# Performance work log

Measured on AMD Instinct MI355X. Metric: run time of the kernel, lower is better.

The kernel has to match this reference:

```python
import jax, jax.numpy as jnp
import numpy as np

B, S, D = 64, 4096, 64          # bsz*n_heads, seq_len, head_size
WINDOW = 256                    # num_toks_attended
NEG = -10000.0


def setup_inputs() -> dict:
    key = jax.random.key(0)
    kq, kk, kv = jax.random.split(key, 3)
    q = jax.random.normal(kq, (B, S, D), dtype=jnp.float32)
    k = jax.random.normal(kk, (B, S, D), dtype=jnp.float32)
    v = jax.random.normal(kv, (B, S, D), dtype=jnp.float32)
    return {"q": q, "k": k, "v": v}


def reference(q, k, v):
    # sliding_window_attn, topk_for_softmax=-1 (plain softmax)
    b, s, d = q.shape
    hw = WINDOW // 2                       # half window = 128
    n = s // hw                            # number of half-window bins
    split = lambda x: x.reshape(b, n, hw, d)
    bq, bk, bv = split(q), split(k), split(v)

    def cat_half_neighbours(x):
        # left-rolled, self, right-rolled half-bins -> [b, n, 3*hw, d]
        return jnp.concatenate(
            (jnp.roll(x, 1, axis=1), x, jnp.roll(x, -1, axis=1)), axis=-2)

    bk = cat_half_neighbours(bk)
    bv = cat_half_neighbours(bv)

    dots = jnp.einsum('bnid,bnjd->bnij', bq, bk) * (d ** -0.5)  # [b,n,hw,3hw]

    # mask: strict lower triangle on left block, none on middle,
    # upper-incl-diagonal on right block (as in the torch code)
    lmask = jnp.tril(jnp.ones((hw, hw), dtype=bool), -1)
    mask = jnp.concatenate((lmask, jnp.zeros_like(lmask), ~lmask), axis=-1)
    dots = jnp.where(mask, NEG, dots)

    p = jax.nn.softmax(dots, axis=-1)
    bo = jnp.einsum('bnij,bnjd->bnid', p, bv)
    return bo.reshape(b, s, d)
```

## Files before the change

### kernel.cpp

```cpp
#include <hip/hip_runtime.h>
#include <hip/hip_bf16.h>
#include <stdint.h>

using f32x4  = __attribute__((ext_vector_type(4))) float;
using bf16x8 = __attribute__((ext_vector_type(8))) __bf16;
using bf16x2 = __attribute__((ext_vector_type(2))) __bf16;
typedef unsigned int u32;

#define SEQ 4096

__global__ __launch_bounds__(256, 2) void lattn_kern(
        const float* __restrict__ Q, const float* __restrict__ K,
        const float* __restrict__ V, float* __restrict__ O)
{
    __shared__ __bf16 Kl[320 * 64];
    __shared__ __bf16 Vt[64 * 320];

    const int tid  = threadIdx.x;
    const int wv   = tid >> 6;
    const int lane = tid & 63;
    const int g    = lane >> 4;
    const int c    = lane & 15;

    const int b    = blockIdx.x >> 3;
    const int oct  = blockIdx.x & 7;
    const size_t baseB = (size_t)b * (SEQ * 64);
    const int t00  = oct * 512;

    int r0 = (t00 + SEQ - 128) % 320;

    #pragma unroll
    for (int it = 0; it < 10; ++it) {
        const int ch = tid + it * 256;
        const int j = ch >> 3, dg = ch & 7;
        const int grow = (t00 - 128 + j) & (SEQ - 1);
        int row = r0 + j; if (row >= 320) row -= 320;
        const float* src = K + baseB + (size_t)grow * 64 + dg * 8;
        f32x4 k0 = *(const f32x4*)src, k1 = *(const f32x4*)(src + 4);
        bf16x8 hk;
        #pragma unroll
        for (int u = 0; u < 4; ++u) { hk[u] = (__bf16)k0[u]; hk[u + 4] = (__bf16)k1[u]; }
        *(bf16x8*)((char*)Kl + row * 128 + (((u32)dg ^ (u32)(row & 7)) << 4)) = hk;
    }
    #pragma unroll
    for (int it = 0; it < 5; ++it) {
        const int ch = tid + it * 256;
        const int rp = ch >> 3, dg = ch & 7;
        const int grow = (t00 - 128 + 2 * rp) & (SEQ - 1);
        int col = r0 + 2 * rp; if (col >= 320) col -= 320;
        const float* src = V + baseB + (size_t)grow * 64 + dg * 8;
        f32x4 a0 = *(const f32x4*)src,        a1 = *(const f32x4*)(src + 4);
        f32x4 b0 = *(const f32x4*)(src + 64), b1 = *(const f32x4*)(src + 68);
        #pragma unroll
        for (int u = 0; u < 8; ++u) {
            const int d = dg * 8 + u;
            bf16x2 pv;
            pv[0] = (__bf16)((u < 4) ? a0[u] : a1[u - 4]);
            pv[1] = (__bf16)((u < 4) ? b0[u] : b1[u - 4]);
            const u32 sw = (u32)(u ^ dg);
            *(bf16x2*)((char*)Vt + (((u32)d * 640u + (u32)col * 2u) ^ (sw << 4))) = pv;
        }
    }

    const u32 swc = (u32)(c & 7);

    for (int i = 0; i < 8; ++i) {
        const int t0 = t00 + i * 64;
        __syncthreads();

        f32x4 dk[4], dv[4];
        int krow0 = 0, krow1 = 0, vcol = 0, kdg = 0, vdg = 0;
        if (i < 7) {
            {
                const int jj = tid >> 3; kdg = tid & 7;
                const int grow0 = (t0 + 192 + jj) & (SEQ - 1);
                const float* s0 = K + baseB + (size_t)grow0 * 64 + kdg * 8;
                dk[0] = *(const f32x4*)s0; dk[1] = *(const f32x4*)(s0 + 4);
                krow0 = r0 + jj;
                const int grow1 = (t0 + 192 + jj + 32) & (SEQ - 1);
                const float* s1 = K + baseB + (size_t)grow1 * 64 + kdg * 8;
                dk[2] = *(const f32x4*)s1; dk[3] = *(const f32x4*)(s1 + 4);
                krow1 = r0 + jj + 32;
            }
            {
                const int rp = tid >> 3; vdg = tid & 7;
                const int grow = (t0 + 192 + 2 * rp) & (SEQ - 1);
                const float* s0 = V + baseB + (size_t)grow * 64 + vdg * 8;
                dv[0] = *(const f32x4*)s0;        dv[1] = *(const f32x4*)(s0 + 4);
                dv[2] = *(const f32x4*)(s0 + 64); dv[3] = *(const f32x4*)(s0 + 68);
                vcol = r0 + 2 * rp;
            }
        }

        bf16x8 aq0, aq1;
        {
            const float* qp = Q + baseB + (size_t)(t0 + wv * 16 + c) * 64 + g * 8;
            f32x4 q0 = *(const f32x4*)qp,        q1 = *(const f32x4*)(qp + 4);
            f32x4 q2 = *(const f32x4*)(qp + 32), q3 = *(const f32x4*)(qp + 36);
            #pragma unroll
            for (int u = 0; u < 4; ++u) {
                aq0[u] = (__bf16)q0[u]; aq0[u + 4] = (__bf16)q1[u];
                aq1[u] = (__bf16)q2[u]; aq1[u + 4] = (__bf16)q3[u];
            }
        }

        f32x4 s_[20];
        const int rc = r0 + c;
        #pragma unroll
        for (int t = 0; t < 20; ++t) {
            if (t >= wv && t <= wv + 16) {
                int row = rc + 16 * t; if (row >= 320) row -= 320;
                const u32 ka = (u32)row * 128u;
                bf16x8 kb0 = *(const bf16x8*)((const char*)Kl + ka + (((u32)g ^ swc) << 4));
                bf16x8 kb1 = *(const bf16x8*)((const char*)Kl + ka + (((u32)(g + 4) ^ swc) << 4));
                f32x4 acc = {0.f, 0.f, 0.f, 0.f};
                __builtin_amdgcn_s_setprio(1);
                acc = __builtin_amdgcn_mfma_f32_16x16x32_bf16(aq0, kb0, acc, 0, 0, 0);
                acc = __builtin_amdgcn_mfma_f32_16x16x32_bf16(aq1, kb1, acc, 0, 0, 0);
                __builtin_amdgcn_s_setprio(0);
                s_[t] = acc;
            } else {
                s_[t] = (f32x4){0.f, 0.f, 0.f, 0.f};
            }
        }
        __syncthreads();

        float sm4[4] = {0.f, 0.f, 0.f, 0.f};
        #pragma unroll
        for (int t = 0; t < 20; ++t) {
            if (t >= wv && t <= wv + 16) {
                #pragma unroll
                for (int r = 0; r < 4; ++r) {
                    float e = __expf(s_[t][r] * 0.125f);
                    if (t == wv)      e = (c <  g * 4 + r) ? 0.f : e;
                    if (t == wv + 16) e = (c >= g * 4 + r) ? 0.f : e;
                    s_[t][r] = e; sm4[r] += e;
                }
            }
        }
        #pragma unroll
        for (int d = 1; d < 16; d <<= 1) {
            #pragma unroll
            for (int r = 0; r < 4; ++r) sm4[r] += __shfl_xor(sm4[r], d, 64);
        }
        float inv[4];
        #pragma unroll
        for (int r = 0; r < 4; ++r) inv[r] = 1.0f / sm4[r];

        char* Pw = (char*)Kl + r0 * 128 + wv * 2048;
        f32x4 o[4] = {{0,0,0,0},{0,0,0,0},{0,0,0,0},{0,0,0,0}};
        #pragma unroll
        for (int c5 = 0; c5 < 5; ++c5) {
            #pragma unroll
            for (int tt = 0; tt < 4; ++tt) {
                const int t = c5 * 4 + tt;
                const bool live = (t >= wv && t <= wv + 16);
                #pragma unroll
                for (int r = 0; r < 4; ++r) {
                    const int prow = g * 4 + r;
                    const u32 pb = ((u32)prow * 128u + (u32)(tt * 16 + c) * 2u)
                                 ^ ((u32)(prow & 7) << 4);
                    float pv_ = live ? s_[t][r] : 0.f;
                    *(__bf16*)(Pw + pb) = (__bf16)pv_;
                }
            }
            #pragma unroll
            for (int kk = 0; kk < 2; ++kk) {
                const u32 pa_b = ((u32)c * 128u + (u32)(kk * 64 + g * 16)) ^ (swc << 4);
                const bf16x8 pa = *(const bf16x8*)(Pw + pa_b);
                int col0 = r0 + c5 * 64 + kk * 32 + g * 8;
                if (col0 >= 320) col0 -= 320;
                __builtin_amdgcn_s_setprio(1);
                #pragma unroll
                for (int dt = 0; dt < 4; ++dt) {
                    const int d  = dt * 16 + c;
                    const u32 sw = (u32)((d & 7) ^ ((d >> 3) & 7));
                    const u32 vb = ((u32)d * 640u + (u32)col0 * 2u) ^ (sw << 4);
                    const bf16x8 bb = *(const bf16x8*)((const char*)Vt + vb);
                    o[dt] = __builtin_amdgcn_mfma_f32_16x16x32_bf16(pa, bb, o[dt], 0, 0, 0);
                }
                __builtin_amdgcn_s_setprio(0);
            }
        }

        #pragma unroll
        for (int dt = 0; dt < 4; ++dt) {
            #pragma unroll
            for (int r = 0; r < 4; ++r) {
                const int row = t0 + wv * 16 + g * 4 + r;
                O[baseB + (size_t)row * 64 + dt * 16 + c] = o[dt][r] * inv[r];
            }
        }

        if (i < 7) {
            __syncthreads();
            bf16x8 hk;
            #pragma unroll
            for (int u = 0; u < 4; ++u) { hk[u] = (__bf16)dk[0][u]; hk[u + 4] = (__bf16)dk[1][u]; }
            *(bf16x8*)((char*)Kl + krow0 * 128 + (((u32)kdg ^ (u32)(krow0 & 7)) << 4)) = hk;
            #pragma unroll
            for (int u = 0; u < 4; ++u) { hk[u] = (__bf16)dk[2][u]; hk[u + 4] = (__bf16)dk[3][u]; }
            *(bf16x8*)((char*)Kl + krow1 * 128 + (((u32)kdg ^ (u32)(krow1 & 7)) << 4)) = hk;
            #pragma unroll
            for (int u = 0; u < 8; ++u) {
                const int d = vdg * 8 + u;
                bf16x2 pv;
                pv[0] = (__bf16)((u < 4) ? dv[0][u] : dv[1][u - 4]);
                pv[1] = (__bf16)((u < 4) ? dv[2][u] : dv[3][u - 4]);
                const u32 sw = (u32)(u ^ vdg);
                *(bf16x2*)((char*)Vt + (((u32)d * 640u + (u32)vcol * 2u) ^ (sw << 4))) = pv;
            }
            r0 += 64; if (r0 >= 320) r0 -= 320;
        }
    }
}

extern "C" void kernel_launch(void* const* d_in, const int* in_sizes, int n_in,
                              void* d_out, int out_size, void* d_ws, size_t ws_size,
                              hipStream_t stream) {
    const float* q = (const float*)d_in[0];
    const float* k = (const float*)d_in[1];
    const float* v = (const float*)d_in[2];
    float* o = (float*)d_out;
    const int nB = in_sizes[0] / (SEQ * 64);
    dim3 grid(nB * 8), block(256);
    hipLaunchKernelGGL(lattn_kern, grid, block, 0, stream, q, k, v, o);
}
```

Baseline: 83.94 us.

## Compute transposed scores so P stays in registers, drop LDS round-trip

```diff
diff --git a/kernel.cpp b/kernel.cpp
--- a/kernel.cpp
+++ b/kernel.cpp
@@ -4,10 +4,16 @@
 
 using f32x4  = __attribute__((ext_vector_type(4))) float;
 using bf16x8 = __attribute__((ext_vector_type(8))) __bf16;
+using bf16x4 = __attribute__((ext_vector_type(4))) __bf16;
 using bf16x2 = __attribute__((ext_vector_type(2))) __bf16;
 typedef unsigned int u32;
 
 #define SEQ 4096
+
+__device__ __forceinline__ void mfma16(f32x4& acc, bf16x4 a, bf16x4 b) {
+    asm volatile("v_mfma_f32_16x16x16_bf16 %0, %1, %2, %0"
+                 : "+v"(acc) : "v"(a), "v"(b));
+}
 
 __global__ __launch_bounds__(256, 2) void lattn_kern(
         const float* __restrict__ Q, const float* __restrict__ K,
@@ -21,6 +27,7 @@
     const int lane = tid & 63;
     const int g    = lane >> 4;
     const int c    = lane & 15;
+    const u32 swc  = (u32)(c & 7);
 
     const int b    = blockIdx.x >> 3;
     const int oct  = blockIdx.x & 7;
@@ -62,15 +69,44 @@
         }
     }
 
-    const u32 swc = (u32)(c & 7);
+    bf16x8 aq0, aq1;
+    {
+        const float* qp = Q + baseB + (size_t)(t00 + wv * 16 + c) * 64 + g * 8;
+        f32x4 q0 = *(const f32x4*)qp,        q1 = *(const f32x4*)(qp + 4);
+        f32x4 q2 = *(const f32x4*)(qp + 32), q3 = *(const f32x4*)(qp + 36);
+        #pragma unroll
+        for (int u = 0; u < 4; ++u) {
+            aq0[u] = (__bf16)q0[u]; aq0[u + 4] = (__bf16)q1[u];
+            aq1[u] = (__bf16)q2[u]; aq1[u + 4] = (__bf16)q3[u];
+        }
+    }
 
     for (int i = 0; i < 8; ++i) {
         const int t0 = t00 + i * 64;
         __syncthreads();
 
-        f32x4 dk[4], dv[4];
+        f32x4 s_[17];
+        const int rb = r0 + 16 * wv + c;
+        __builtin_amdgcn_s_setprio(1);
+        #pragma unroll
+        for (int lt = 0; lt < 17; ++lt) {
+            int row = rb + 16 * lt; if (row >= 320) row -= 320;
+            const char* ka = (const char*)Kl + (u32)row * 128u;
+            bf16x8 a0 = *(const bf16x8*)(ka + (((u32)g ^ swc) << 4));
+            bf16x8 a1 = *(const bf16x8*)(ka + (((u32)(g + 4) ^ swc) << 4));
+            f32x4 acc = {0.f, 0.f, 0.f, 0.f};
+            acc = __builtin_amdgcn_mfma_f32_16x16x32_bf16(a0, aq0, acc, 0, 0, 0);
+            acc = __builtin_amdgcn_mfma_f32_16x16x32_bf16(a1, aq1, acc, 0, 0, 0);
+            s_[lt] = acc;
+        }
+        __builtin_amdgcn_s_setprio(0);
+
+        f32x4 qn0, qn1, qn2, qn3, dk[4], dv[4];
         int krow0 = 0, krow1 = 0, vcol = 0, kdg = 0, vdg = 0;
         if (i < 7) {
+            const float* qp = Q + baseB + (size_t)(t0 + 64 + wv * 16 + c) * 64 + g * 8;
+            qn0 = *(const f32x4*)qp;        qn1 = *(const f32x4*)(qp + 4);
+            qn2 = *(const f32x4*)(qp + 32); qn3 = *(const f32x4*)(qp + 36);
             {
                 const int jj = tid >> 3; kdg = tid & 7;
                 const int grow0 = (t0 + 192 + jj) & (SEQ - 1);
@@ -92,103 +128,53 @@
             }
         }
 
-        bf16x8 aq0, aq1;
-        {
-            const float* qp = Q + baseB + (size_t)(t0 + wv * 16 + c) * 64 + g * 8;
-            f32x4 q0 = *(const f32x4*)qp,        q1 = *(const f32x4*)(qp + 4);
-            f32x4 q2 = *(const f32x4*)(qp + 32), q3 = *(const f32x4*)(qp + 36);
-            #pragma unroll
-            for (int u = 0; u < 4; ++u) {
-                aq0[u] = (__bf16)q0[u]; aq0[u + 4] = (__bf16)q1[u];
-                aq1[u] = (__bf16)q2[u]; aq1[u + 4] = (__bf16)q3[u];
-            }
-        }
-
-        f32x4 s_[20];
-        const int rc = r0 + c;
-        #pragma unroll
-        for (int t = 0; t < 20; ++t) {
-            if (t >= wv && t <= wv + 16) {
-                int row = rc + 16 * t; if (row >= 320) row -= 320;
-                const u32 ka = (u32)row * 128u;
-                bf16x8 kb0 = *(const bf16x8*)((const char*)Kl + ka + (((u32)g ^ swc) << 4));
-                bf16x8 kb1 = *(const bf16x8*)((const char*)Kl + ka + (((u32)(g + 4) ^ swc) << 4));
-                f32x4 acc = {0.f, 0.f, 0.f, 0.f};
-                __builtin_amdgcn_s_setprio(1);
-                acc = __builtin_amdgcn_mfma_f32_16x16x32_bf16(aq0, kb0, acc, 0, 0, 0);
-                acc = __builtin_amdgcn_mfma_f32_16x16x32_bf16(aq1, kb1, acc, 0, 0, 0);
-                __builtin_amdgcn_s_setprio(0);
-                s_[t] = acc;
-            } else {
-                s_[t] = (f32x4){0.f, 0.f, 0.f, 0.f};
-            }
-        }
-        __syncthreads();
-
-        float sm4[4] = {0.f, 0.f, 0.f, 0.f};
-        #pragma unroll
-        for (int t = 0; t < 20; ++t) {
-            if (t >= wv && t <= wv + 16) {
-                #pragma unroll
-                for (int r = 0; r < 4; ++r) {
-                    float e = __expf(s_[t][r] * 0.125f);
-                    if (t == wv)      e = (c <  g * 4 + r) ? 0.f : e;
-                    if (t == wv + 16) e = (c >= g * 4 + r) ? 0.f : e;
-                    s_[t][r] = e; sm4[r] += e;
-                }
-            }
-        }
-        #pragma unroll
-        for (int d = 1; d < 16; d <<= 1) {
-            #pragma unroll
-            for (int r = 0; r < 4; ++r) sm4[r] += __shfl_xor(sm4[r], d, 64);
-        }
-        float inv[4];
-        #pragma unroll
-        for (int r = 0; r < 4; ++r) inv[r] = 1.0f / sm4[r];
-
-        char* Pw = (char*)Kl + r0 * 128 + wv * 2048;
+        const int k4 = 4 * g;
+        float sum = 0.f;
+        #pragma unroll
+        for (int lt = 0; lt < 17; ++lt) {
+            #pragma unroll
+            for (int r = 0; r < 4; ++r) {
+                float e = exp2f(s_[lt][r] * 0.18033688f);
+                if (lt == 0)  e = (k4 + r <  c) ? 0.f : e;
+                if (lt == 16) e = (k4 + r >= c) ? 0.f : e;
+                s_[lt][r] = e; sum += e;
+            }
+        }
+        sum += __shfl_xor(sum, 16, 64);
+        sum += __shfl_xor(sum, 32, 64);
+        const float inv = 1.0f / sum;
+
+        bf16x4 pa[17];
+        #pragma unroll
+        for (int lt = 0; lt < 17; ++lt) {
+            #pragma unroll
+            for (int r = 0; r < 4; ++r) pa[lt][r] = (__bf16)(s_[lt][r] * inv);
+        }
+
         f32x4 o[4] = {{0,0,0,0},{0,0,0,0},{0,0,0,0},{0,0,0,0}};
-        #pragma unroll
-        for (int c5 = 0; c5 < 5; ++c5) {
-            #pragma unroll
-            for (int tt = 0; tt < 4; ++tt) {
-                const int t = c5 * 4 + tt;
-                const bool live = (t >= wv && t <= wv + 16);
-                #pragma unroll
-                for (int r = 0; r < 4; ++r) {
-                    const int prow = g * 4 + r;
-                    const u32 pb = ((u32)prow * 128u + (u32)(tt * 16 + c) * 2u)
-                                 ^ ((u32)(prow & 7) << 4);
-                    float pv_ = live ? s_[t][r] : 0.f;
-                    *(__bf16*)(Pw + pb) = (__bf16)pv_;
-                }
-            }
-            #pragma unroll
-            for (int kk = 0; kk < 2; ++kk) {
-                const u32 pa_b = ((u32)c * 128u + (u32)(kk * 64 + g * 16)) ^ (swc << 4);
-                const bf16x8 pa = *(const bf16x8*)(Pw + pa_b);
-                int col0 = r0 + c5 * 64 + kk * 32 + g * 8;
-                if (col0 >= 320) col0 -= 320;
-                __builtin_amdgcn_s_setprio(1);
-                #pragma unroll
-                for (int dt = 0; dt < 4; ++dt) {
-                    const int d  = dt * 16 + c;
-                    const u32 sw = (u32)((d & 7) ^ ((d >> 3) & 7));
-                    const u32 vb = ((u32)d * 640u + (u32)col0 * 2u) ^ (sw << 4);
-                    const bf16x8 bb = *(const bf16x8*)((const char*)Vt + vb);
-                    o[dt] = __builtin_amdgcn_mfma_f32_16x16x32_bf16(pa, bb, o[dt], 0, 0, 0);
-                }
-                __builtin_amdgcn_s_setprio(0);
-            }
-        }
+        const int cb = r0 + 16 * wv + 4 * g;
+        __builtin_amdgcn_s_setprio(1);
+        #pragma unroll
+        for (int lt = 0; lt < 17; ++lt) {
+            int col = cb + 16 * lt; if (col >= 320) col -= 320;
+            #pragma unroll
+            for (int dt = 0; dt < 4; ++dt) {
+                const int d  = dt * 16 + c;
+                const u32 sw = (u32)((d & 7) ^ ((d >> 3) & 7));
+                const u32 vb = ((u32)d * 640u + (u32)col * 2u) ^ (sw << 4);
+                const bf16x4 vbf = *(const bf16x4*)((const char*)Vt + vb);
+                mfma16(o[dt], pa[lt], vbf);
+            }
+        }
+        __builtin_amdgcn_s_setprio(0);
+        asm volatile("s_nop 7\n\ts_nop 7" ::);
 
         #pragma unroll
         for (int dt = 0; dt < 4; ++dt) {
             #pragma unroll
             for (int r = 0; r < 4; ++r) {
-                const int row = t0 + wv * 16 + g * 4 + r;
-                O[baseB + (size_t)row * 64 + dt * 16 + c] = o[dt][r] * inv[r];
+                const int row = t0 + wv * 16 + 4 * g + r;
+                O[baseB + (size_t)row * 64 + dt * 16 + c] = o[dt][r];
             }
         }
 
@@ -211,6 +197,11 @@
                 *(bf16x2*)((char*)Vt + (((u32)d * 640u + (u32)vcol * 2u) ^ (sw << 4))) = pv;
             }
             r0 += 64; if (r0 >= 320) r0 -= 320;
+            #pragma unroll
+            for (int u = 0; u < 4; ++u) {
+                aq0[u] = (__bf16)qn0[u]; aq0[u + 4] = (__bf16)qn1[u];
+                aq1[u] = (__bf16)qn2[u]; aq1[u + 4] = (__bf16)qn3[u];
+            }
         }
     }
 }
```

Measured after the change: 71.69 us. 14.6% less time.
